# Performance work log

Hardware: AMD Instinct MI355X
Metric: run time of the kernel (lower is better)

The kernel has to match this reference:

```python
import jax, jax.numpy as jnp
import numpy as np

N = 20000      # num nodes
E = 320000     # num edges (avg degree 16)
F_IN = 518     # object_feature_dim
D = 128        # node_embedding_dim (= GAT out_channels)
ED = 32        # edge_embedding_dim
R = 26         # num_relations
H = 4          # GAT heads (concat=False -> mean over heads)
HID = 256      # node_encoder hidden


def _gat_layer(x, src, dst, ea, lin, lin_e, att_s, att_d, att_e, bias):
    """PyG GATConv: add_self_loops=True (fill_value='mean'), concat=False, negative_slope=0.2."""
    n = x.shape[0]
    ones = jnp.ones((src.shape[0],), x.dtype)
    cnt = jax.ops.segment_sum(ones, dst, num_segments=n)                    # [N]
    loop_ea = jax.ops.segment_sum(ea, dst, num_segments=n) / jnp.maximum(cnt, 1.0)[:, None]
    idx = jnp.arange(n)
    s = jnp.concatenate([src, idx])
    d = jnp.concatenate([dst, idx])
    ea2 = jnp.concatenate([ea, loop_ea], axis=0)                            # [E+N, ED]
    h = (x @ lin).reshape(n, H, D)                                          # [N,H,D]
    a_s = jnp.einsum('nhd,hd->nh', h, att_s)                                # [N,H]
    a_d = jnp.einsum('nhd,hd->nh', h, att_d)
    e = (ea2 @ lin_e).reshape(-1, H, D)                                     # [E+N,H,D]
    a_e = jnp.einsum('ehd,hd->eh', e, att_e)
    alpha = jax.nn.leaky_relu(a_s[s] + a_d[d] + a_e, 0.2)                   # [E+N,H]
    amax = jax.ops.segment_max(alpha, d, num_segments=n)
    alpha = jnp.exp(alpha - amax[d])
    denom = jax.ops.segment_sum(alpha, d, num_segments=n)
    alpha = alpha / (denom[d] + 1e-16)                                      # segment softmax
    msg = h[s] * alpha[:, :, None]                                          # [E+N,H,D]
    out = jax.ops.segment_sum(msg, d, num_segments=n)                       # [N,H,D]
    return out.mean(axis=1) + bias                                          # concat=False


def setup_inputs() -> dict:
    key = jax.random.key(0)
    ks = jax.random.split(key, 18)
    g = lambda k, shp, s=0.05: jax.random.normal(k, shp, jnp.float32) * s
    return {
        'x': g(ks[0], (N, F_IN), 1.0),
        'edge_index': jax.random.randint(ks[1], (2, E), 0, N),
        'edge_type': jax.random.randint(ks[2], (E,), 0, R),
        'w1': g(ks[3], (F_IN, HID)), 'b1': jnp.zeros((HID,), jnp.float32),
        'w2': g(ks[4], (HID, D)),    'b2': jnp.zeros((D,), jnp.float32),
        'rel_emb': g(ks[5], (R, ED), 1.0),
        'lin1': g(ks[6], (D, H * D)), 'line1': g(ks[7], (ED, H * D)),
        'atts1': g(ks[8], (H, D)), 'attd1': g(ks[9], (H, D)), 'atte1': g(ks[10], (H, D)),
        'bias1': jnp.zeros((D,), jnp.float32),
        'lin2': g(ks[11], (D, H * D)), 'line2': g(ks[12], (ED, H * D)),
        'atts2': g(ks[13], (H, D)), 'attd2': g(ks[14], (H, D)), 'atte2': g(ks[15], (H, D)),
        'bias2': jnp.zeros((D,), jnp.float32),
    }


def reference(x, edge_index, edge_type, w1, b1, w2, b2, rel_emb,
              lin1, line1, atts1, attd1, atte1, bias1,
              lin2, line2, atts2, attd2, atte2, bias2):
    src, dst = edge_index[0], edge_index[1]
    # node encoder (dropout inactive in eval)
    h = jax.nn.relu(x @ w1 + b1) @ w2 + b2                                  # [N,D]
    ea = rel_emb[edge_type]                                                 # [E,ED]
    h = jax.nn.relu(_gat_layer(h, src, dst, ea, lin1, line1, atts1, attd1, atte1, bias1))
    h = jax.nn.relu(_gat_layer(h, src, dst, ea, lin2, line2, atts2, attd2, atte2, bias2))
    return h
```

## Files before the change

kernel.cpp:

```cpp
#include <hip/hip_runtime.h>
#include <math.h>

#define N_NODES 20000
#define MP      20032
#define N_EDGES 320000
#define F_IN    518
#define HIDDEN  256
#define DIM     128
#define NH      4

typedef __attribute__((ext_vector_type(8))) short bf16x8;
typedef __attribute__((ext_vector_type(4))) float f32x4;
typedef unsigned short ushort_t;

__device__ __forceinline__ float lrelu02(float x) { return x > 0.f ? x : 0.2f * x; }

__device__ __forceinline__ void gl_lds16(const void* g, void* l) {
    __builtin_amdgcn_global_load_lds(
        (const __attribute__((address_space(1))) unsigned int*)g,
        (__attribute__((address_space(3))) unsigned int*)l, 16, 0, 0);
}

__device__ __forceinline__ unsigned int hi16(float v) { return __float_as_uint(v) >> 16; }
__device__ __forceinline__ unsigned int lo16(float v) {
    unsigned int h = __float_as_uint(v) & 0xFFFF0000u;
    return __float_as_uint(v - __uint_as_float(h)) >> 16;
}
__device__ __forceinline__ unsigned int rnd16(float v) {
    unsigned int u = __float_as_uint(v);
    return (u + 0x7FFFu + ((u >> 16) & 1u)) >> 16;
}
__device__ __forceinline__ float bfl(unsigned int u) { return __uint_as_float(u << 16); }
__device__ __forceinline__ float bfh(unsigned int u) { return __uint_as_float(u & 0xFFFF0000u); }

__global__ __launch_bounds__(256, 4) void gemm_mfma_v2(
    const ushort_t* __restrict__ Ah, const ushort_t* __restrict__ Al,
    const ushort_t* __restrict__ Bh, const ushort_t* __restrict__ Bl,
    const float* __restrict__ bias,
    int M, int K8, int N, int act,
    float* __restrict__ Cf, ushort_t* __restrict__ Ch, ushort_t* __restrict__ Cl,
    ushort_t* __restrict__ Cb)
{
    __shared__ __align__(16) ushort_t lds[12288];
    const int tid = threadIdx.x;
    const int w = tid >> 6, lane = tid & 63;
    const int row0 = blockIdx.y * 64, col0 = blockIdx.x * 128;
    const int nkb = K8 >> 2;
    const int m16 = lane & 15, q = lane >> 4;

    f32x4 acc[4][2] = {};

    for (int kb = 0; kb < nkb; ++kb) {
        const size_t kc = (size_t)(kb * 4 + w);
        const size_t aoff = (kc * MP + row0) * 8 + lane * 8;
        const size_t boff = (kc * N + col0) * 8 + lane * 8;
        gl_lds16(Ah + aoff, &lds[w * 512]);
        gl_lds16(Al + aoff, &lds[2048 + w * 512]);
        gl_lds16(Bh + boff,       &lds[4096 + w * 1024]);
        gl_lds16(Bh + boff + 512, &lds[4096 + w * 1024 + 512]);
        gl_lds16(Bl + boff,       &lds[8192 + w * 1024]);
        gl_lds16(Bl + boff + 512, &lds[8192 + w * 1024 + 512]);
        __syncthreads();

        bf16x8 fah[4], fal[4], fbh[2], fbl[2];
        const int fa = q * 512 + m16 * 8;
        #pragma unroll
        for (int mi = 0; mi < 4; ++mi) {
            fah[mi] = *(const bf16x8*)&lds[fa + mi * 128];
            fal[mi] = *(const bf16x8*)&lds[2048 + fa + mi * 128];
        }
        const int fb = q * 1024 + (w * 32 + m16) * 8;
        #pragma unroll
        for (int ni = 0; ni < 2; ++ni) {
            fbh[ni] = *(const bf16x8*)&lds[4096 + fb + ni * 128];
            fbl[ni] = *(const bf16x8*)&lds[8192 + fb + ni * 128];
        }
        #pragma unroll
        for (int mi = 0; mi < 4; ++mi)
            #pragma unroll
            for (int ni = 0; ni < 2; ++ni) {
                acc[mi][ni] = __builtin_amdgcn_mfma_f32_16x16x32_bf16(fah[mi], fbh[ni], acc[mi][ni], 0, 0, 0);
                acc[mi][ni] = __builtin_amdgcn_mfma_f32_16x16x32_bf16(fah[mi], fbl[ni], acc[mi][ni], 0, 0, 0);
                acc[mi][ni] = __builtin_amdgcn_mfma_f32_16x16x32_bf16(fal[mi], fbh[ni], acc[mi][ni], 0, 0, 0);
            }
        __syncthreads();
    }

    #pragma unroll
    for (int ni = 0; ni < 2; ++ni) {
        const int col = col0 + w * 32 + ni * 16 + m16;
        const float bb = bias ? bias[col] : 0.f;
        #pragma unroll
        for (int mi = 0; mi < 4; ++mi) {
            #pragma unroll
            for (int r = 0; r < 4; ++r) {
                const int row = row0 + mi * 16 + q * 4 + r;
                if (row < M) {
                    float v = acc[mi][ni][r] + bb;
                    if (act) v = fmaxf(v, 0.f);
                    if (Cf) Cf[(size_t)row * N + col] = v;
                    if (Cb) Cb[(size_t)row * N + col] = (ushort_t)rnd16(v);
                    if (Ch) {
                        const size_t p = (((size_t)(col >> 3)) * MP + row) * 8 + (col & 7);
                        Ch[p] = (ushort_t)hi16(v);
                        Cl[p] = (ushort_t)lo16(v);
                    }
                }
            }
        }
    }
}

__global__ __launch_bounds__(256) void conv_a_kernel(
    const float* __restrict__ x, ushort_t* __restrict__ xh, ushort_t* __restrict__ xl)
{
    const int row = blockIdx.x * 256 + threadIdx.x;
    const int k8 = blockIdx.y;
    if (row >= MP) return;
    float v[8];
    #pragma unroll
    for (int j = 0; j < 8; ++j) {
        const int k = k8 * 8 + j;
        v[j] = (row < N_NODES && k < F_IN) ? x[(size_t)row * F_IN + k] : 0.f;
    }
    unsigned int hp[4], lp[4];
    #pragma unroll
    for (int i = 0; i < 4; ++i) {
        hp[i] = (hi16(v[2*i+1]) << 16) | hi16(v[2*i]);
        lp[i] = (lo16(v[2*i+1]) << 16) | lo16(v[2*i]);
    }
    const size_t p = ((size_t)k8 * MP + row) * 8;
    *(uint4*)(xh + p) = make_uint4(hp[0], hp[1], hp[2], hp[3]);
    *(uint4*)(xl + p) = make_uint4(lp[0], lp[1], lp[2], lp[3]);
}

__global__ __launch_bounds__(256) void conv_b_kernel(
    const float* __restrict__ w, ushort_t* __restrict__ bh, ushort_t* __restrict__ bl,
    int K, int N, int total)
{
    const int idx = blockIdx.x * 256 + threadIdx.x;
    if (idx >= total) return;
    const int j = idx & 7;
    const int rem = idx >> 3;
    const int n = rem % N;
    const int k = (rem / N) * 8 + j;
    const float v = (k < K) ? w[(size_t)k * N + n] : 0.f;
    bh[idx] = (ushort_t)hi16(v);
    bl[idx] = (ushort_t)lo16(v);
}

__global__ __launch_bounds__(256) void wa_kernel(
    const float* __restrict__ lin, const float* __restrict__ atts,
    const float* __restrict__ attd, float* __restrict__ wa_s, float* __restrict__ wa_d)
{
    const int wrk = blockIdx.x * 256 + threadIdx.x;
    if (wrk >= 1024) return;
    const int sd = wrk >> 9;
    const int p = wrk & 511;
    const int h = p >> 7, d = p & 127;
    const float* av = (sd ? attd : atts) + h * DIM;
    const float* lp = lin + (size_t)d * (NH * DIM) + h * DIM;
    float acc = 0.f;
    #pragma unroll 8
    for (int i = 0; i < DIM; ++i) acc += lp[i] * av[i];
    (sd ? wa_d : wa_s)[h * DIM + d] = acc;
}

__global__ __launch_bounds__(256) void as_ad_kernel(
    const float* __restrict__ xb, const float* __restrict__ wa_s,
    const float* __restrict__ wa_d, float* __restrict__ a_s, float* __restrict__ a_d)
{
    const int gw = blockIdx.x * 4 + (threadIdx.x >> 6);
    const int lane = threadIdx.x & 63;
    if (gw >= N_NODES * NH) return;
    const int n = gw >> 2, h = gw & 3;
    const float* hp = xb + (size_t)n * DIM;
    float2 hv = *(const float2*)(hp + lane * 2);
    float2 sv = *(const float2*)(wa_s + h * DIM + lane * 2);
    float2 dv = *(const float2*)(wa_d + h * DIM + lane * 2);
    float s = hv.x * sv.x + hv.y * sv.y;
    float d = hv.x * dv.x + hv.y * dv.y;
    #pragma unroll
    for (int off = 32; off > 0; off >>= 1) {
        s += __shfl_down(s, off);
        d += __shfl_down(d, off);
    }
    if (lane == 0) { a_s[n * 4 + h] = s; a_d[n * 4 + h] = d; }
}

__global__ __launch_bounds__(128) void rel_table_kernel(
    const float* __restrict__ rel_emb, const float* __restrict__ line,
    const float* __restrict__ atte, float* __restrict__ table)
{
    __shared__ float we[32][NH];
    const int tid = threadIdx.x;
    const int k = tid >> 2, h = tid & 3;
    float acc = 0.f;
    for (int d = 0; d < DIM; ++d)
        acc += line[(size_t)k * (NH * DIM) + h * DIM + d] * atte[h * DIM + d];
    we[k][h] = acc;
    __syncthreads();
    if (tid < 26 * NH) {
        int r = tid >> 2, hh = tid & 3;
        float t = 0.f;
        for (int kk = 0; kk < 32; ++kk) t += rel_emb[r * 32 + kk] * we[kk][hh];
        table[r * 4 + hh] = t;
    }
}

__global__ __launch_bounds__(256) void hist_kernel(
    const int* __restrict__ dst, int* __restrict__ cnt)
{
    const int e = blockIdx.x * blockDim.x + threadIdx.x;
    if (e >= N_EDGES) return;
    atomicAdd(&cnt[dst[e]], 1);
}

__global__ __launch_bounds__(1024) void scan_kernel(
    const int* __restrict__ cnt, int* __restrict__ ptr, int* __restrict__ ptr_copy)
{
    __shared__ int tsum[1024];
    const int tid = threadIdx.x;
    const int CH = 20;
    const int base = tid * CH;
    int s = 0;
    #pragma unroll
    for (int i = 0; i < CH; ++i) {
        int idx = base + i;
        if (idx < N_NODES) s += cnt[idx];
    }
    tsum[tid] = s;
    __syncthreads();
    for (int off = 1; off < 1024; off <<= 1) {
        int v = (tid >= off) ? tsum[tid - off] : 0;
        __syncthreads();
        tsum[tid] += v;
        __syncthreads();
    }
    int run = (tid == 0) ? 0 : tsum[tid - 1];
    #pragma unroll
    for (int i = 0; i < CH; ++i) {
        int idx = base + i;
        if (idx < N_NODES) {
            ptr[idx] = run;
            ptr_copy[idx] = run;
            run += cnt[idx];
        }
    }
    if (tid == 0) ptr[N_NODES] = N_EDGES;
}

__global__ __launch_bounds__(256) void scatter_kernel(
    const int* __restrict__ src, const int* __restrict__ dst, const int* __restrict__ etype,
    int* __restrict__ ptr_copy, int2* __restrict__ se)
{
    const int e = blockIdx.x * blockDim.x + threadIdx.x;
    if (e >= N_EDGES) return;
    const int d = dst[e];
    const int pos = atomicAdd(&ptr_copy[d], 1);
    se[pos] = make_int2(src[e], etype[e]);
}

__global__ __launch_bounds__(256) void node_agg_kernel(
    const int* __restrict__ ptr, const int2* __restrict__ se,
    const float* __restrict__ a_s, const float* __restrict__ a_d,
    const float* __restrict__ table, const ushort_t* __restrict__ hb,
    const float* __restrict__ bias,
    float* __restrict__ outf, ushort_t* __restrict__ oh, ushort_t* __restrict__ ol)
{
    const int n = blockIdx.x * 4 + (threadIdx.x >> 6);
    const int lane = threadIdx.x & 63;
    if (n >= N_NODES) return;
    const int beg = ptr[n], end = ptr[n + 1];
    const int head = lane >> 4;
    const int cbase = lane * 8;

    const float4 ad4 = *(const float4*)(a_d + n * 4);
    float acc[8] = {};
    float d0 = 0, d1 = 0, d2 = 0, d3 = 0;
    float e0 = 0, e1 = 0, e2 = 0, e3 = 0;

    int j = beg;
    for (; j + 2 <= end; j += 2) {
        const int2 E0 = se[j], E1 = se[j + 1];
        const uint4 g0 = *(const uint4*)(hb + (size_t)E0.x * 512 + cbase);
        const uint4 g1 = *(const uint4*)(hb + (size_t)E1.x * 512 + cbase);
        const float4 as0 = *(const float4*)(a_s + E0.x * 4);
        const float4 tv0 = *(const float4*)(table + E0.y * 4);
        const float4 as1 = *(const float4*)(a_s + E1.x * 4);
        const float4 tv1 = *(const float4*)(table + E1.y * 4);
        const float p00 = __expf(lrelu02(as0.x + ad4.x + tv0.x));
        const float p01 = __expf(lrelu02(as0.y + ad4.y + tv0.y));
        const float p02 = __expf(lrelu02(as0.z + ad4.z + tv0.z));
        const float p03 = __expf(lrelu02(as0.w + ad4.w + tv0.w));
        const float p10 = __expf(lrelu02(as1.x + ad4.x + tv1.x));
        const float p11 = __expf(lrelu02(as1.y + ad4.y + tv1.y));
        const float p12 = __expf(lrelu02(as1.z + ad4.z + tv1.z));
        const float p13 = __expf(lrelu02(as1.w + ad4.w + tv1.w));
        e0 += tv0.x + tv1.x; e1 += tv0.y + tv1.y;
        e2 += tv0.z + tv1.z; e3 += tv0.w + tv1.w;
        d0 += p00 + p10; d1 += p01 + p11; d2 += p02 + p12; d3 += p03 + p13;
        const float w0 = head < 2 ? (head == 0 ? p00 : p01) : (head == 2 ? p02 : p03);
        const float w1 = head < 2 ? (head == 0 ? p10 : p11) : (head == 2 ? p12 : p13);
        acc[0] += w0 * bfl(g0.x) + w1 * bfl(g1.x);
        acc[1] += w0 * bfh(g0.x) + w1 * bfh(g1.x);
        acc[2] += w0 * bfl(g0.y) + w1 * bfl(g1.y);
        acc[3] += w0 * bfh(g0.y) + w1 * bfh(g1.y);
        acc[4] += w0 * bfl(g0.z) + w1 * bfl(g1.z);
        acc[5] += w0 * bfh(g0.z) + w1 * bfh(g1.z);
        acc[6] += w0 * bfl(g0.w) + w1 * bfl(g1.w);
        acc[7] += w0 * bfh(g0.w) + w1 * bfh(g1.w);
    }
    if (j < end) {
        const int2 E0 = se[j];
        const uint4 g0 = *(const uint4*)(hb + (size_t)E0.x * 512 + cbase);
        const float4 as0 = *(const float4*)(a_s + E0.x * 4);
        const float4 tv0 = *(const float4*)(table + E0.y * 4);
        const float p00 = __expf(lrelu02(as0.x + ad4.x + tv0.x));
        const float p01 = __expf(lrelu02(as0.y + ad4.y + tv0.y));
        const float p02 = __expf(lrelu02(as0.z + ad4.z + tv0.z));
        const float p03 = __expf(lrelu02(as0.w + ad4.w + tv0.w));
        e0 += tv0.x; e1 += tv0.y; e2 += tv0.z; e3 += tv0.w;
        d0 += p00; d1 += p01; d2 += p02; d3 += p03;
        const float w0 = head < 2 ? (head == 0 ? p00 : p01) : (head == 2 ? p02 : p03);
        acc[0] += w0 * bfl(g0.x); acc[1] += w0 * bfh(g0.x);
        acc[2] += w0 * bfl(g0.y); acc[3] += w0 * bfh(g0.y);
        acc[4] += w0 * bfl(g0.z); acc[5] += w0 * bfh(g0.z);
        acc[6] += w0 * bfl(g0.w); acc[7] += w0 * bfh(g0.w);
    }

    const float inv = 1.0f / fmaxf((float)(end - beg), 1.0f);
    const float4 asn = *(const float4*)(a_s + n * 4);
    {
        const float p0 = __expf(lrelu02(asn.x + ad4.x + e0 * inv));
        const float p1 = __expf(lrelu02(asn.y + ad4.y + e1 * inv));
        const float p2 = __expf(lrelu02(asn.z + ad4.z + e2 * inv));
        const float p3 = __expf(lrelu02(asn.w + ad4.w + e3 * inv));
        d0 += p0; d1 += p1; d2 += p2; d3 += p3;
        const uint4 g0 = *(const uint4*)(hb + (size_t)n * 512 + cbase);
        const float w0 = head < 2 ? (head == 0 ? p0 : p1) : (head == 2 ? p2 : p3);
        acc[0] += w0 * bfl(g0.x); acc[1] += w0 * bfh(g0.x);
        acc[2] += w0 * bfl(g0.y); acc[3] += w0 * bfh(g0.y);
        acc[4] += w0 * bfl(g0.z); acc[5] += w0 * bfh(g0.z);
        acc[6] += w0 * bfl(g0.w); acc[7] += w0 * bfh(g0.w);
    }

    const float i0 = 0.25f / (d0 + 1e-16f);
    const float i1 = 0.25f / (d1 + 1e-16f);
    const float i2 = 0.25f / (d2 + 1e-16f);
    const float i3 = 0.25f / (d3 + 1e-16f);
    const float ih = head < 2 ? (head == 0 ? i0 : i1) : (head == 2 ? i2 : i3);
    float t[8];
    #pragma unroll
    for (int k = 0; k < 8; ++k) {
        t[k] = acc[k] * ih;
        t[k] += __shfl_xor(t[k], 16);
        t[k] += __shfl_xor(t[k], 32);
    }
    if (lane < 16) {
        const float4 b0 = *(const float4*)(bias + cbase);
        const float4 b1 = *(const float4*)(bias + cbase + 4);
        float o[8];
        o[0] = fmaxf(t[0] + b0.x, 0.f); o[1] = fmaxf(t[1] + b0.y, 0.f);
        o[2] = fmaxf(t[2] + b0.z, 0.f); o[3] = fmaxf(t[3] + b0.w, 0.f);
        o[4] = fmaxf(t[4] + b1.x, 0.f); o[5] = fmaxf(t[5] + b1.y, 0.f);
        o[6] = fmaxf(t[6] + b1.z, 0.f); o[7] = fmaxf(t[7] + b1.w, 0.f);
        if (outf) {
            float4 v0 = {o[0], o[1], o[2], o[3]};
            float4 v1 = {o[4], o[5], o[6], o[7]};
            *(float4*)(outf + (size_t)n * DIM + cbase) = v0;
            *(float4*)(outf + (size_t)n * DIM + cbase + 4) = v1;
        }
        if (oh) {
            unsigned int hp[4], lp[4];
            #pragma unroll
            for (int i = 0; i < 4; ++i) {
                hp[i] = (hi16(o[2*i+1]) << 16) | hi16(o[2*i]);
                lp[i] = (lo16(o[2*i+1]) << 16) | lo16(o[2*i]);
            }
            const size_t p = ((size_t)lane * MP + n) * 8;
            *(uint4*)(oh + p) = make_uint4(hp[0], hp[1], hp[2], hp[3]);
            *(uint4*)(ol + p) = make_uint4(lp[0], lp[1], lp[2], lp[3]);
        }
    }
}

extern "C" void kernel_launch(void* const* d_in, const int* in_sizes, int n_in,
                              void* d_out, int out_size, void* d_ws, size_t ws_size,
                              hipStream_t stream)
{
    const float* x       = (const float*)d_in[0];
    const int*   eidx    = (const int*)d_in[1];
    const int*   etype   = (const int*)d_in[2];
    const float* w1      = (const float*)d_in[3];
    const float* b1      = (const float*)d_in[4];
    const float* w2      = (const float*)d_in[5];
    const float* b2      = (const float*)d_in[6];
    const float* rel_emb = (const float*)d_in[7];
    const float* lin[2]  = {(const float*)d_in[8],  (const float*)d_in[14]};
    const float* line[2] = {(const float*)d_in[9],  (const float*)d_in[15]};
    const float* atts[2] = {(const float*)d_in[10], (const float*)d_in[16]};
    const float* attd[2] = {(const float*)d_in[11], (const float*)d_in[17]};
    const float* atte[2] = {(const float*)d_in[12], (const float*)d_in[18]};
    const float* bias[2] = {(const float*)d_in[13], (const float*)d_in[19]};
    const int* src = eidx;
    const int* dst = eidx + N_EDGES;

    char* base = (char*)d_ws;
    size_t off = 0;
    auto alloc = [&](size_t bytes) -> void* {
        void* p = base + off;
        off = (off + bytes + 255) & ~(size_t)255;
        return p;
    };
    ushort_t* xh  = (ushort_t*)alloc((size_t)68 * MP * 8 * 2);
    ushort_t* xl  = (ushort_t*)alloc((size_t)68 * MP * 8 * 2);
    ushort_t* h1h = (ushort_t*)alloc((size_t)32 * MP * 8 * 2);
    ushort_t* h1l = (ushort_t*)alloc((size_t)32 * MP * 8 * 2);
    ushort_t* x0h = (ushort_t*)alloc((size_t)16 * MP * 8 * 2);
    ushort_t* x0l = (ushort_t*)alloc((size_t)16 * MP * 8 * 2);
    void* reg1    = alloc((size_t)16 * MP * 8 * 2 * 2);
    ushort_t* w1h = (ushort_t*)alloc(68 * 256 * 8 * 2);
    ushort_t* w1l = (ushort_t*)alloc(68 * 256 * 8 * 2);
    ushort_t* w2h = (ushort_t*)alloc(32 * 128 * 8 * 2);
    ushort_t* w2l = (ushort_t*)alloc(32 * 128 * 8 * 2);
    ushort_t* l0h = (ushort_t*)alloc(16 * 512 * 8 * 2);
    ushort_t* l0l = (ushort_t*)alloc(16 * 512 * 8 * 2);
    ushort_t* l1h = (ushort_t*)alloc(16 * 512 * 8 * 2);
    ushort_t* l1l = (ushort_t*)alloc(16 * 512 * 8 * 2);
    float* a_s   = (float*)alloc(N_NODES * 4 * 4);
    float* a_d   = (float*)alloc(N_NODES * 4 * 4);
    float* table = (float*)alloc(128 * 4);
    float* wa_s  = (float*)alloc(512 * 4);
    float* wa_d  = (float*)alloc(512 * 4);
    int*  cnt_i  = (int*)alloc(N_NODES * 4);
    int*  ptr    = (int*)alloc((N_NODES + 4) * 4);
    int*  ptrc   = (int*)alloc(N_NODES * 4);
    int2* se     = (int2*)alloc((size_t)N_EDGES * 8);

    ushort_t* hb = xh;
    float* xbuf1 = (float*)h1h;
    float* xbuf0 = (float*)reg1;
    ushort_t* x1h = (ushort_t*)reg1;
    ushort_t* x1l = x1h + (size_t)16 * MP * 8;

    const int mtiles = MP / 64;

    conv_a_kernel<<<dim3((MP + 255) / 256, 68), 256, 0, stream>>>(x, xh, xl);
    conv_b_kernel<<<(68*256*8 + 255) / 256, 256, 0, stream>>>(w1, w1h, w1l, F_IN, HIDDEN, 68*256*8);
    conv_b_kernel<<<(32*128*8 + 255) / 256, 256, 0, stream>>>(w2, w2h, w2l, HIDDEN, DIM, 32*128*8);
    conv_b_kernel<<<(16*512*8 + 255) / 256, 256, 0, stream>>>(lin[0], l0h, l0l, DIM, NH*DIM, 16*512*8);
    conv_b_kernel<<<(16*512*8 + 255) / 256, 256, 0, stream>>>(lin[1], l1h, l1l, DIM, NH*DIM, 16*512*8);

    hipMemsetAsync(cnt_i, 0, N_NODES * sizeof(int), stream);
    hist_kernel<<<(N_EDGES + 255) / 256, 256, 0, stream>>>(dst, cnt_i);
    scan_kernel<<<1, 1024, 0, stream>>>(cnt_i, ptr, ptrc);
    scatter_kernel<<<(N_EDGES + 255) / 256, 256, 0, stream>>>(src, dst, etype, ptrc, se);

    gemm_mfma_v2<<<dim3(HIDDEN / 128, mtiles), 256, 0, stream>>>(
        xh, xl, w1h, w1l, b1, N_NODES, 68, HIDDEN, 1, nullptr, h1h, h1l, nullptr);
    gemm_mfma_v2<<<dim3(DIM / 128, mtiles), 256, 0, stream>>>(
        h1h, h1l, w2h, w2l, b2, N_NODES, 32, DIM, 0, xbuf0, x0h, x0l, nullptr);

    gemm_mfma_v2<<<dim3((NH * DIM) / 128, mtiles), 256, 0, stream>>>(
        x0h, x0l, l0h, l0l, nullptr, N_NODES, 16, NH * DIM, 0, nullptr, nullptr, nullptr, hb);
    wa_kernel<<<4, 256, 0, stream>>>(lin[0], atts[0], attd[0], wa_s, wa_d);
    as_ad_kernel<<<N_NODES, 256, 0, stream>>>(xbuf0, wa_s, wa_d, a_s, a_d);
    rel_table_kernel<<<1, 128, 0, stream>>>(rel_emb, line[0], atte[0], table);
    node_agg_kernel<<<(N_NODES + 3) / 4, 256, 0, stream>>>(
        ptr, se, a_s, a_d, table, hb, bias[0], xbuf1, x1h, x1l);

    gemm_mfma_v2<<<dim3((NH * DIM) / 128, mtiles), 256, 0, stream>>>(
        x1h, x1l, l1h, l1l, nullptr, N_NODES, 16, NH * DIM, 0, nullptr, nullptr, nullptr, hb);
    wa_kernel<<<4, 256, 0, stream>>>(lin[1], atts[1], attd[1], wa_s, wa_d);
    as_ad_kernel<<<N_NODES, 256, 0, stream>>>(xbuf1, wa_s, wa_d, a_s, a_d);
    rel_table_kernel<<<1, 128, 0, stream>>>(rel_emb, line[1], atte[1], table);
    node_agg_kernel<<<(N_NODES + 3) / 4, 256, 0, stream>>>(
        ptr, se, a_s, a_d, table, hb, bias[1], (float*)d_out, nullptr, nullptr);
}
```

Measured before the change: 495.5 us.

## Use single rounded bf16 A operand for GAT linear GEMMs and simplify per-head aggregation

The GAT-layer linear GEMMs now take the activation as one round-to-nearest bf16 array instead of a hi/lo split pair. This drops one of the three MFMA passes and the A-low loads, and the producers (second encoder GEMM and the layer-1 aggregation) now write a single bf16 array. The node aggregation kernel also stops computing all four heads' exponentials per lane and computes only its own head, with scalar gathers of a_s and table entries. The cost is lower input precision on those GEMMs, which could affect accuracy.

```diff
diff --git a/kernel.cpp b/kernel.cpp
--- a/kernel.cpp
+++ b/kernel.cpp
@@ -38,8 +38,10 @@
     const ushort_t* __restrict__ Bh, const ushort_t* __restrict__ Bl,
     const float* __restrict__ bias,
     int M, int K8, int N, int act,
-    float* __restrict__ Cf, ushort_t* __restrict__ Ch, ushort_t* __restrict__ Cl,
-    ushort_t* __restrict__ Cb)
+    float* __restrict__ Cf,
+    ushort_t* __restrict__ Ch, ushort_t* __restrict__ Cl,
+    ushort_t* __restrict__ Cb,
+    ushort_t* __restrict__ Ca)
 {
     __shared__ __align__(16) ushort_t lds[12288];
     const int tid = threadIdx.x;
@@ -47,6 +49,7 @@
     const int row0 = blockIdx.y * 64, col0 = blockIdx.x * 128;
     const int nkb = K8 >> 2;
     const int m16 = lane & 15, q = lane >> 4;
+    const bool use_al = (Al != nullptr);
 
     f32x4 acc[4][2] = {};
 
@@ -55,7 +58,7 @@
         const size_t aoff = (kc * MP + row0) * 8 + lane * 8;
         const size_t boff = (kc * N + col0) * 8 + lane * 8;
         gl_lds16(Ah + aoff, &lds[w * 512]);
-        gl_lds16(Al + aoff, &lds[2048 + w * 512]);
+        if (use_al) gl_lds16(Al + aoff, &lds[2048 + w * 512]);
         gl_lds16(Bh + boff,       &lds[4096 + w * 1024]);
         gl_lds16(Bh + boff + 512, &lds[4096 + w * 1024 + 512]);
         gl_lds16(Bl + boff,       &lds[8192 + w * 1024]);
@@ -67,7 +70,7 @@
         #pragma unroll
         for (int mi = 0; mi < 4; ++mi) {
             fah[mi] = *(const bf16x8*)&lds[fa + mi * 128];
-            fal[mi] = *(const bf16x8*)&lds[2048 + fa + mi * 128];
+            if (use_al) fal[mi] = *(const bf16x8*)&lds[2048 + fa + mi * 128];
         }
         const int fb = q * 1024 + (w * 32 + m16) * 8;
         #pragma unroll
@@ -81,8 +84,14 @@
             for (int ni = 0; ni < 2; ++ni) {
                 acc[mi][ni] = __builtin_amdgcn_mfma_f32_16x16x32_bf16(fah[mi], fbh[ni], acc[mi][ni], 0, 0, 0);
                 acc[mi][ni] = __builtin_amdgcn_mfma_f32_16x16x32_bf16(fah[mi], fbl[ni], acc[mi][ni], 0, 0, 0);
-                acc[mi][ni] = __builtin_amdgcn_mfma_f32_16x16x32_bf16(fal[mi], fbh[ni], acc[mi][ni], 0, 0, 0);
             }
+        if (use_al) {
+            #pragma unroll
+            for (int mi = 0; mi < 4; ++mi)
+                #pragma unroll
+                for (int ni = 0; ni < 2; ++ni)
+                    acc[mi][ni] = __builtin_amdgcn_mfma_f32_16x16x32_bf16(fal[mi], fbh[ni], acc[mi][ni], 0, 0, 0);
+        }
         __syncthreads();
     }
 
@@ -100,11 +109,9 @@
                     if (act) v = fmaxf(v, 0.f);
                     if (Cf) Cf[(size_t)row * N + col] = v;
                     if (Cb) Cb[(size_t)row * N + col] = (ushort_t)rnd16(v);
-                    if (Ch) {
-                        const size_t p = (((size_t)(col >> 3)) * MP + row) * 8 + (col & 7);
-                        Ch[p] = (ushort_t)hi16(v);
-                        Cl[p] = (ushort_t)lo16(v);
-                    }
+                    const size_t p = (((size_t)(col >> 3)) * MP + row) * 8 + (col & 7);
+                    if (Ch) { Ch[p] = (ushort_t)hi16(v); Cl[p] = (ushort_t)lo16(v); }
+                    if (Ca) Ca[p] = (ushort_t)rnd16(v);
                 }
             }
         }
@@ -266,7 +273,7 @@
     const float* __restrict__ a_s, const float* __restrict__ a_d,
     const float* __restrict__ table, const ushort_t* __restrict__ hb,
     const float* __restrict__ bias,
-    float* __restrict__ outf, ushort_t* __restrict__ oh, ushort_t* __restrict__ ol)
+    float* __restrict__ outf, ushort_t* __restrict__ oa)
 {
     const int n = blockIdx.x * 4 + (threadIdx.x >> 6);
     const int lane = threadIdx.x & 63;
@@ -274,82 +281,59 @@
     const int beg = ptr[n], end = ptr[n + 1];
     const int head = lane >> 4;
     const int cbase = lane * 8;
-
-    const float4 ad4 = *(const float4*)(a_d + n * 4);
+    const float adh = a_d[n * 4 + head];
+
     float acc[8] = {};
-    float d0 = 0, d1 = 0, d2 = 0, d3 = 0;
-    float e0 = 0, e1 = 0, e2 = 0, e3 = 0;
+    float dh = 0.f, eh = 0.f;
 
     int j = beg;
     for (; j + 2 <= end; j += 2) {
         const int2 E0 = se[j], E1 = se[j + 1];
         const uint4 g0 = *(const uint4*)(hb + (size_t)E0.x * 512 + cbase);
         const uint4 g1 = *(const uint4*)(hb + (size_t)E1.x * 512 + cbase);
-        const float4 as0 = *(const float4*)(a_s + E0.x * 4);
-        const float4 tv0 = *(const float4*)(table + E0.y * 4);
-        const float4 as1 = *(const float4*)(a_s + E1.x * 4);
-        const float4 tv1 = *(const float4*)(table + E1.y * 4);
-        const float p00 = __expf(lrelu02(as0.x + ad4.x + tv0.x));
-        const float p01 = __expf(lrelu02(as0.y + ad4.y + tv0.y));
-        const float p02 = __expf(lrelu02(as0.z + ad4.z + tv0.z));
-        const float p03 = __expf(lrelu02(as0.w + ad4.w + tv0.w));
-        const float p10 = __expf(lrelu02(as1.x + ad4.x + tv1.x));
-        const float p11 = __expf(lrelu02(as1.y + ad4.y + tv1.y));
-        const float p12 = __expf(lrelu02(as1.z + ad4.z + tv1.z));
-        const float p13 = __expf(lrelu02(as1.w + ad4.w + tv1.w));
-        e0 += tv0.x + tv1.x; e1 += tv0.y + tv1.y;
-        e2 += tv0.z + tv1.z; e3 += tv0.w + tv1.w;
-        d0 += p00 + p10; d1 += p01 + p11; d2 += p02 + p12; d3 += p03 + p13;
-        const float w0 = head < 2 ? (head == 0 ? p00 : p01) : (head == 2 ? p02 : p03);
-        const float w1 = head < 2 ? (head == 0 ? p10 : p11) : (head == 2 ? p12 : p13);
-        acc[0] += w0 * bfl(g0.x) + w1 * bfl(g1.x);
-        acc[1] += w0 * bfh(g0.x) + w1 * bfh(g1.x);
-        acc[2] += w0 * bfl(g0.y) + w1 * bfl(g1.y);
-        acc[3] += w0 * bfh(g0.y) + w1 * bfh(g1.y);
-        acc[4] += w0 * bfl(g0.z) + w1 * bfl(g1.z);
-        acc[5] += w0 * bfh(g0.z) + w1 * bfh(g1.z);
-        acc[6] += w0 * bfl(g0.w) + w1 * bfl(g1.w);
-        acc[7] += w0 * bfh(g0.w) + w1 * bfh(g1.w);
+        const float a0 = a_s[E0.x * 4 + head];
+        const float t0 = table[E0.y * 4 + head];
+        const float a1 = a_s[E1.x * 4 + head];
+        const float t1 = table[E1.y * 4 + head];
+        const float p0 = __expf(lrelu02(a0 + adh + t0));
+        const float p1 = __expf(lrelu02(a1 + adh + t1));
+        eh += t0 + t1;
+        dh += p0 + p1;
+        acc[0] += p0 * bfl(g0.x) + p1 * bfl(g1.x);
+        acc[1] += p0 * bfh(g0.x) + p1 * bfh(g1.x);
+        acc[2] += p0 * bfl(g0.y) + p1 * bfl(g1.y);
+        acc[3] += p0 * bfh(g0.y) + p1 * bfh(g1.y);
+        acc[4] += p0 * bfl(g0.z) + p1 * bfl(g1.z);
+        acc[5] += p0 * bfh(g0.z) + p1 * bfh(g1.z);
+        acc[6] += p0 * bfl(g0.w) + p1 * bfl(g1.w);
+        acc[7] += p0 * bfh(g0.w) + p1 * bfh(g1.w);
     }
     if (j < end) {
         const int2 E0 = se[j];
         const uint4 g0 = *(const uint4*)(hb + (size_t)E0.x * 512 + cbase);
-        const float4 as0 = *(const float4*)(a_s + E0.x * 4);
-        const float4 tv0 = *(const float4*)(table + E0.y * 4);
-        const float p00 = __expf(lrelu02(as0.x + ad4.x + tv0.x));
-        const float p01 = __expf(lrelu02(as0.y + ad4.y + tv0.y));
-        const float p02 = __expf(lrelu02(as0.z + ad4.z + tv0.z));
-        const float p03 = __expf(lrelu02(as0.w + ad4.w + tv0.w));
-        e0 += tv0.x; e1 += tv0.y; e2 += tv0.z; e3 += tv0.w;
-        d0 += p00; d1 += p01; d2 += p02; d3 += p03;
-        const float w0 = head < 2 ? (head == 0 ? p00 : p01) : (head == 2 ? p02 : p03);
-        acc[0] += w0 * bfl(g0.x); acc[1] += w0 * bfh(g0.x);
-        acc[2] += w0 * bfl(g0.y); acc[3] += w0 * bfh(g0.y);
-        acc[4] += w0 * bfl(g0.z); acc[5] += w0 * bfh(g0.z);
-        acc[6] += w0 * bfl(g0.w); acc[7] += w0 * bfh(g0.w);
+        const float a0 = a_s[E0.x * 4 + head];
+        const float t0 = table[E0.y * 4 + head];
+        const float p0 = __expf(lrelu02(a0 + adh + t0));
+        eh += t0;
+        dh += p0;
+        acc[0] += p0 * bfl(g0.x); acc[1] += p0 * bfh(g0.x);
+        acc[2] += p0 * bfl(g0.y); acc[3] += p0 * bfh(g0.y);
+        acc[4] += p0 * bfl(g0.z); acc[5] += p0 * bfh(g0.z);
+        acc[6] += p0 * bfl(g0.w); acc[7] += p0 * bfh(g0.w);
     }
 
     const float inv = 1.0f / fmaxf((float)(end - beg), 1.0f);
-    const float4 asn = *(const float4*)(a_s + n * 4);
+    const float ps = __expf(lrelu02(a_s[n * 4 + head] + adh + eh * inv));
+    dh += ps;
     {
-        const float p0 = __expf(lrelu02(asn.x + ad4.x + e0 * inv));
-        const float p1 = __expf(lrelu02(asn.y + ad4.y + e1 * inv));
-        const float p2 = __expf(lrelu02(asn.z + ad4.z + e2 * inv));
-        const float p3 = __expf(lrelu02(asn.w + ad4.w + e3 * inv));
-        d0 += p0; d1 += p1; d2 += p2; d3 += p3;
-        const uint4 g0 = *(const uint4*)(hb + (size_t)n * 512 + cbase);
-        const float w0 = head < 2 ? (head == 0 ? p0 : p1) : (head == 2 ? p2 : p3);
-        acc[0] += w0 * bfl(g0.x); acc[1] += w0 * bfh(g0.x);
-        acc[2] += w0 * bfl(g0.y); acc[3] += w0 * bfh(g0.y);
-        acc[4] += w0 * bfl(g0.z); acc[5] += w0 * bfh(g0.z);
-        acc[6] += w0 * bfl(g0.w); acc[7] += w0 * bfh(g0.w);
-    }
-
-    const float i0 = 0.25f / (d0 + 1e-16f);
-    const float i1 = 0.25f / (d1 + 1e-16f);
-    const float i2 = 0.25f / (d2 + 1e-16f);
-    const float i3 = 0.25f / (d3 + 1e-16f);
-    const float ih = head < 2 ? (head == 0 ? i0 : i1) : (head == 2 ? i2 : i3);
+        const uint4 gs = *(const uint4*)(hb + (size_t)n * 512 + cbase);
+        acc[0] += ps * bfl(gs.x); acc[1] += ps * bfh(gs.x);
+        acc[2] += ps * bfl(gs.y); acc[3] += ps * bfh(gs.y);
+        acc[4] += ps * bfl(gs.z); acc[5] += ps * bfh(gs.z);
+        acc[6] += ps * bfl(gs.w); acc[7] += ps * bfh(gs.w);
+    }
+
+    const float ih = 0.25f / (dh + 1e-16f);
     float t[8];
     #pragma unroll
     for (int k = 0; k < 8; ++k) {
@@ -371,16 +355,12 @@
             *(float4*)(outf + (size_t)n * DIM + cbase) = v0;
             *(float4*)(outf + (size_t)n * DIM + cbase + 4) = v1;
         }
-        if (oh) {
-            unsigned int hp[4], lp[4];
+        if (oa) {
+            unsigned int up[4];
             #pragma unroll
-            for (int i = 0; i < 4; ++i) {
-                hp[i] = (hi16(o[2*i+1]) << 16) | hi16(o[2*i]);
-                lp[i] = (lo16(o[2*i+1]) << 16) | lo16(o[2*i]);
-            }
-            const size_t p = ((size_t)lane * MP + n) * 8;
-            *(uint4*)(oh + p) = make_uint4(hp[0], hp[1], hp[2], hp[3]);
-            *(uint4*)(ol + p) = make_uint4(lp[0], lp[1], lp[2], lp[3]);
+            for (int i = 0; i < 4; ++i)
+                up[i] = (rnd16(o[2*i+1]) << 16) | rnd16(o[2*i]);
+            *(uint4*)(oa + ((size_t)lane * MP + n) * 8) = make_uint4(up[0], up[1], up[2], up[3]);
         }
     }
 }
@@ -417,9 +397,8 @@
     ushort_t* xl  = (ushort_t*)alloc((size_t)68 * MP * 8 * 2);
     ushort_t* h1h = (ushort_t*)alloc((size_t)32 * MP * 8 * 2);
     ushort_t* h1l = (ushort_t*)alloc((size_t)32 * MP * 8 * 2);
-    ushort_t* x0h = (ushort_t*)alloc((size_t)16 * MP * 8 * 2);
-    ushort_t* x0l = (ushort_t*)alloc((size_t)16 * MP * 8 * 2);
-    void* reg1    = alloc((size_t)16 * MP * 8 * 2 * 2);
+    ushort_t* x0a = (ushort_t*)alloc((size_t)16 * MP * 8 * 2);
+    void* reg1    = alloc((size_t)16 * MP * 8 * 4);
     ushort_t* w1h = (ushort_t*)alloc(68 * 256 * 8 * 2);
     ushort_t* w1l = (ushort_t*)alloc(68 * 256 * 8 * 2);
     ushort_t* w2h = (ushort_t*)alloc(32 * 128 * 8 * 2);
@@ -441,8 +420,7 @@
     ushort_t* hb = xh;
     float* xbuf1 = (float*)h1h;
     float* xbuf0 = (float*)reg1;
-    ushort_t* x1h = (ushort_t*)reg1;
-    ushort_t* x1l = x1h + (size_t)16 * MP * 8;
+    ushort_t* x1a = (ushort_t*)reg1;
 
     const int mtiles = MP / 64;
 
@@ -458,23 +436,23 @@
     scatter_kernel<<<(N_EDGES + 255) / 256, 256, 0, stream>>>(src, dst, etype, ptrc, se);
 
     gemm_mfma_v2<<<dim3(HIDDEN / 128, mtiles), 256, 0, stream>>>(
-        xh, xl, w1h, w1l, b1, N_NODES, 68, HIDDEN, 1, nullptr, h1h, h1l, nullptr);
+        xh, xl, w1h, w1l, b1, N_NODES, 68, HIDDEN, 1, nullptr, h1h, h1l, nullptr, nullptr);
     gemm_mfma_v2<<<dim3(DIM / 128, mtiles), 256, 0, stream>>>(
-        h1h, h1l, w2h, w2l, b2, N_NODES, 32, DIM, 0, xbuf0, x0h, x0l, nullptr);
+        h1h, h1l, w2h, w2l, b2, N_NODES, 32, DIM, 0, xbuf0, nullptr, nullptr, nullptr, x0a);
 
     gemm_mfma_v2<<<dim3((NH * DIM) / 128, mtiles), 256, 0, stream>>>(
-        x0h, x0l, l0h, l0l, nullptr, N_NODES, 16, NH * DIM, 0, nullptr, nullptr, nullptr, hb);
+        x0a, nullptr, l0h, l0l, nullptr, N_NODES, 16, NH * DIM, 0, nullptr, nullptr, nullptr, hb, nullptr);
     wa_kernel<<<4, 256, 0, stream>>>(lin[0], atts[0], attd[0], wa_s, wa_d);
     as_ad_kernel<<<N_NODES, 256, 0, stream>>>(xbuf0, wa_s, wa_d, a_s, a_d);
     rel_table_kernel<<<1, 128, 0, stream>>>(rel_emb, line[0], atte[0], table);
     node_agg_kernel<<<(N_NODES + 3) / 4, 256, 0, stream>>>(
-        ptr, se, a_s, a_d, table, hb, bias[0], xbuf1, x1h, x1l);
+        ptr, se, a_s, a_d, table, hb, bias[0], xbuf1, x1a);
 
     gemm_mfma_v2<<<dim3((NH * DIM) / 128, mtiles), 256, 0, stream>>>(
-        x1h, x1l, l1h, l1l, nullptr, N_NODES, 16, NH * DIM, 0, nullptr, nullptr, nullptr, hb);
+        x1a, nullptr, l1h, l1l, nullptr, N_NODES, 16, NH * DIM, 0, nullptr, nullptr, nullptr, hb, nullptr);
     wa_kernel<<<4, 256, 0, stream>>>(lin[1], atts[1], attd[1], wa_s, wa_d);
     as_ad_kernel<<<N_NODES, 256, 0, stream>>>(xbuf1, wa_s, wa_d, a_s, a_d);
     rel_table_kernel<<<1, 128, 0, stream>>>(rel_emb, line[1], atte[1], table);
     node_agg_kernel<<<(N_NODES + 3) / 4, 256, 0, stream>>>(
-        ptr, se, a_s, a_d, table, hb, bias[1], (float*)d_out, nullptr, nullptr);
-}
+        ptr, se, a_s, a_d, table, hb, bias[1], (float*)d_out, nullptr);
+}
```

Result: faster. 473.3 us (-4.5%).
